# Kernel optimization log

Hardware: AMD Instinct MI355X
Metric: run time of the kernel (lower is better)

## Reference

```python
import jax, jax.numpy as jnp
import numpy as np
from jax import lax

TAU = 2.0      # LIF decay constant (source: tau = 2.0)
V_TH = 1.0     # spikingjelly LIFNode default threshold
ALPHA = 2.0    # ATan surrogate default alpha
BN_EPS = 1e-5


@jax.custom_vjp
def spike(v):
    # Heaviside with ATan surrogate gradient (spikingjelly surrogate.ATan)
    return (v >= V_TH).astype(v.dtype)

def _spike_fwd(v):
    return spike(v), v

def _spike_bwd(v, g):
    x = (jnp.pi / 2.0) * ALPHA * (v - V_TH)
    return (g * (ALPHA / 2.0) / (1.0 + x * x),)

spike.defvjp(_spike_fwd, _spike_bwd)


def lif_step(v, x):
    # leaky integrate: v += (x - (v - v_reset)) / tau, v_reset = 0
    v = v + (x - v) / TAU
    s = spike(v)
    # hard reset to 0; detach_reset=True -> stop_gradient on s in the reset path
    v = v * (1.0 - lax.stop_gradient(s))
    return v, s


def multistep_lif(x_seq):
    # x_seq: (T, ...) ; membrane state carried across T, initial v = 0
    v0 = jnp.zeros_like(x_seq[0])
    _, s_seq = lax.scan(lif_step, v0, x_seq)
    return s_seq


def setup_inputs() -> dict:
    key = jax.random.key(0)
    ks = jax.random.split(key, 3)
    bs, length, c_num, hidden = 64, 128, 32, 256
    x = jax.random.normal(ks[0], (bs, length, c_num), dtype=jnp.float32)
    conv_w = jax.random.normal(ks[1], (hidden, 1, 1, 3), dtype=jnp.float32) * 0.3
    conv_b = jnp.zeros((hidden,), jnp.float32)
    bn_gamma = jnp.ones((hidden,), jnp.float32)
    bn_beta = jnp.zeros((hidden,), jnp.float32)
    bn_mean = jnp.zeros((hidden,), jnp.float32)
    bn_var = jnp.ones((hidden,), jnp.float32)
    lin_w = jax.random.normal(ks[2], (hidden, hidden), dtype=jnp.float32) * (1.0 / np.sqrt(hidden))
    lin_b = jnp.zeros((hidden,), jnp.float32)
    return {"x": x, "conv_w": conv_w, "conv_b": conv_b, "bn_gamma": bn_gamma,
            "bn_beta": bn_beta, "bn_mean": bn_mean, "bn_var": bn_var,
            "lin_w": lin_w, "lin_b": lin_b}


def reference(x, conv_w, conv_b, bn_gamma, bn_beta, bn_mean, bn_var, lin_w, lin_b):
    bs, length, c_num = x.shape
    hidden = conv_w.shape[0]

    # ---- ConvEncoder ----
    xi = jnp.transpose(x, (0, 2, 1))[:, None]  # (bs, 1, c_num, length)
    enc = lax.conv_general_dilated(
        xi, conv_w, window_strides=(1, 1), padding=((0, 0), (1, 1)),
        dimension_numbers=("NCHW", "OIHW", "NCHW"))
    enc = enc + conv_b[None, :, None, None]
    # BatchNorm2d (eval mode, running stats)
    inv = bn_gamma * lax.rsqrt(bn_var + BN_EPS)
    enc = (enc - bn_mean[None, :, None, None]) * inv[None, :, None, None] + bn_beta[None, :, None, None]
    # multi-step LIF over channel dim T = hidden (as in source permute(1,0,2,3))
    enc = jnp.transpose(enc, (1, 0, 2, 3))          # (hidden, bs, c_num, length)
    spks_enc = multistep_lif(enc)                   # (hidden, bs, c_num, length)

    # ---- reshape to per-(bs*c_num) sequences of length `length` with feature hidden ----
    h = jnp.transpose(spks_enc, (1, 2, 3, 0)).reshape(bs * c_num, length, hidden)

    # ---- SpikeRNNCell recurrence over time (Linear + stateful LIF) ----
    def rnn_step(v, x_t):                           # x_t: (N, hidden)
        z = x_t @ lin_w.T + lin_b
        v = v + (z - v) / TAU
        s = spike(v)
        v = v * (1.0 - lax.stop_gradient(s))
        return v, s

    v0 = jnp.zeros((bs * c_num, hidden), x.dtype)
    _, s_seq = lax.scan(rnn_step, v0, jnp.transpose(h, (1, 0, 2)))  # (length, N, hidden)
    spks = s_seq[-1]                                # final-step spikes (N, hidden)

    spks = spks.reshape(bs, c_num * hidden, -1)     # (bs, c_num*hidden, 1)
    return jnp.transpose(spks, (0, 2, 1)), spks[:, :, -1]
```

## Files before the change

kernel.cpp:

```cpp
#include <hip/hip_runtime.h>
#include <stdint.h>

typedef unsigned short u16;
typedef unsigned int u32;
typedef unsigned long long u64;
typedef unsigned char u8;

typedef __attribute__((ext_vector_type(4))) int   i32x4;
typedef __attribute__((ext_vector_type(8))) int   i32x8;
typedef __attribute__((ext_vector_type(4))) float f32x4;
typedef __attribute__((ext_vector_type(2))) float f32x2;

#define OFF_SBITS 0u
#define SBITS_BYTES (2048u * 128u * 32u)
#define OFF_WQ4  (SBITS_BYTES)
#define WQ4_BYTES (2u * 32768u)
#define OFF_SCL  (OFF_WQ4 + WQ4_BYTES)

__global__ __launch_bounds__(256) void prep_enc_kernel(
    const float* __restrict__ x,
    const float* __restrict__ conv_w, const float* __restrict__ conv_b,
    const float* __restrict__ gamma,  const float* __restrict__ beta,
    const float* __restrict__ mean,   const float* __restrict__ var,
    const float* __restrict__ lin_w,  uint8_t* __restrict__ ws,
    u64* __restrict__ sbits) {
    int tid = threadIdx.x;
    int blk = blockIdx.x;
    if (blk < 256) {
        __shared__ float red[256];
        __shared__ u8 nib[256];
        int j = blk, k = tid;
        float wv = lin_w[j * 256 + k];
        red[k] = fabsf(wv);
        __syncthreads();
        #pragma unroll
        for (int s = 128; s > 0; s >>= 1) {
            if (k < s) red[k] = fmaxf(red[k], red[k + s]);
            __syncthreads();
        }
        float m = red[0];
        float S = (m > 0.f) ? 6.0f / m : 0.f;
        float v6 = wv * S;
        float av = fabsf(v6);
        int code;
        if      (av < 0.25f) code = 0;
        else if (av < 0.75f) code = 1;
        else if (av < 1.25f) code = 2;
        else if (av < 1.75f) code = 3;
        else if (av < 2.5f)  code = 4;
        else if (av < 3.5f)  code = 5;
        else if (av < 5.0f)  code = 6;
        else                 code = 7;
        nib[k] = (u8)(((v6 < 0.f && code) ? 8 : 0) | code);
        __syncthreads();
        if (k < 128) {
            u8 byte = (u8)(nib[2 * k] | (nib[2 * k + 1] << 4));
            int ks = k >> 6, kb = (k >> 4) & 3, bi = k & 15;
            (ws + OFF_WQ4)[ks * 32768 + (j * 4 + kb) * 16 + bi] = byte;
        }
        if (k == 0) ((float*)(ws + OFF_SCL))[j] = m * (1.0f / 12.0f);
    } else {
        __shared__ float4 cfl[256];
        {
            int h = tid;
            float inv = gamma[h] / sqrtf(var[h] + 1e-5f);
            float K = (conv_b[h] - mean[h]) * inv + beta[h];
            cfl[h] = make_float4(conv_w[h * 3 + 0] * inv * 0.5f,
                                 conv_w[h * 3 + 1] * inv * 0.5f,
                                 conv_w[h * 3 + 2] * inv * 0.5f, K * 0.5f);
        }
        int p = (blk - 256) * 256 + tid;
        int c = p & 31;
        int l = (p >> 5) & 127;
        int b0 = p >> 12;
        int xb = b0 * 4096 + l * 32 + c;
        float xb0 = x[xb],            xb1 = x[xb + 131072];
        float xa0 = (l > 0)   ? x[xb - 32]          : 0.f;
        float xa1 = (l > 0)   ? x[xb + 131072 - 32] : 0.f;
        float xc0 = (l < 127) ? x[xb + 32]          : 0.f;
        float xc1 = (l < 127) ? x[xb + 131072 + 32] : 0.f;
        u64* d0 = sbits + ((size_t)(b0 * 32 + c) * 128 + (size_t)l) * 4;
        u64* d1 = d0 + (size_t)1024 * 512;

        f32x2 XA = {xa0, xa1};
        f32x2 XB = {xb0, xb1};
        f32x2 XC = {xc0, xc1};
        const f32x2 half2 = {0.5f, 0.5f};

        __syncthreads();
        f32x2 v2 = {0.f, 0.f};
        u64 cur0 = 0ull, cur1 = 0ull;
        #pragma unroll 8
        for (int h = 0; h < 256; ++h) {
            float4 a = cfl[h];
            f32x2 ax = {a.x, a.x};
            f32x2 ay = {a.y, a.y};
            f32x2 az = {a.z, a.z};
            f32x2 aw = {a.w, a.w};
            f32x2 e = __builtin_elementwise_fma(az, XC, aw);
            e = __builtin_elementwise_fma(ay, XB, e);
            e = __builtin_elementwise_fma(ax, XA, e);
            v2 = __builtin_elementwise_fma(half2, v2, e);
            bool s0 = (v2.x >= 1.0f);
            bool s1 = (v2.y >= 1.0f);
            cur0 |= ((u64)(s0 ? 1u : 0u)) << (h & 63);
            cur1 |= ((u64)(s1 ? 1u : 0u)) << (h & 63);
            if ((h & 63) == 63) {
                d0[h >> 6] = cur0; d1[h >> 6] = cur1;
                cur0 = 0ull; cur1 = 0ull;
            }
            v2.x = s0 ? 0.f : v2.x;
            v2.y = s1 ? 0.f : v2.y;
        }
    }
}

__device__ __forceinline__ u32 nib_perm(u32 byte) {
    u32 t1 = byte | (byte << 6);
    u32 t2 = t1 | (t1 << 12);
    u32 sel = t2 & 0x03030303u;
    return __builtin_amdgcn_perm(0x22200200u, 0x22200200u, sel);
}

__global__ __launch_bounds__(256, 2) void gemm_scan_kernel(
    const u64* __restrict__ sbits,
    const uint4* __restrict__ wq4,
    const float* __restrict__ lin_b,
    const float* __restrict__ sclp,
    float* __restrict__ out) {
    __shared__ __align__(16) uint8_t smem[36864];
    u32* Awords = (u32*)smem;

    int tid  = threadIdx.x;
    int n    = blockIdx.x;
    int lane = tid & 63;
    int w    = tid >> 6;
    int l15  = lane & 15;
    int quad = lane >> 4;
    int lb   = w * 256 + l15 * 4 + quad;

    float bias = lin_b[tid];
    float sc   = sclp[tid];

    i32x4 bb[2][4];
    #pragma unroll
    for (int ks = 0; ks < 2; ++ks)
        #pragma unroll
        for (int nf = 0; nf < 4; ++nf)
            bb[ks][nf] = ((const i32x4*)wq4)[(size_t)(ks * 2048 + nf * 64 + lb)];

    __builtin_amdgcn_global_load_lds(
        (const __attribute__((address_space(1))) u32*)
            ((const u64*)sbits + (size_t)n * 512 + tid * 2),
        (__attribute__((address_space(3))) u32*)(smem + w * 1024), 16, 0, 0);

    f32x4 acc[8][4];
    #pragma unroll
    for (int mf = 0; mf < 8; ++mf)
        #pragma unroll
        for (int nf = 0; nf < 4; ++nf) {
            f32x4 z = {0.f, 0.f, 0.f, 0.f};
            acc[mf][nf] = z;
        }

    __syncthreads();

    u32 aw[8][2];
    #pragma unroll
    for (int mf = 0; mf < 8; ++mf)
        #pragma unroll
        for (int ks = 0; ks < 2; ++ks)
            aw[mf][ks] = Awords[(mf * 16 + l15) * 8 + ks * 4 + quad];

    i32x8 afr;
    afr[4] = 0; afr[5] = 0; afr[6] = 0; afr[7] = 0;

    #pragma unroll
    for (int ks = 0; ks < 2; ++ks) {
        i32x8 bfr[4];
        #pragma unroll
        for (int nf = 0; nf < 4; ++nf) {
            bfr[nf][0] = bb[ks][nf][0]; bfr[nf][1] = bb[ks][nf][1];
            bfr[nf][2] = bb[ks][nf][2]; bfr[nf][3] = bb[ks][nf][3];
            bfr[nf][4] = 0; bfr[nf][5] = 0; bfr[nf][6] = 0; bfr[nf][7] = 0;
        }
        #pragma unroll
        for (int mf = 0; mf < 8; ++mf) {
            u32 wbits = aw[mf][ks];
            afr[0] = (int)nib_perm(wbits & 0xFFu);
            afr[1] = (int)nib_perm((wbits >> 8) & 0xFFu);
            afr[2] = (int)nib_perm((wbits >> 16) & 0xFFu);
            afr[3] = (int)nib_perm(wbits >> 24);
            #pragma unroll
            for (int nf = 0; nf < 4; ++nf) {
                acc[mf][nf] = __builtin_amdgcn_mfma_scale_f32_16x16x128_f8f6f4(
                    afr, bfr[nf], acc[mf][nf], 4, 4,
                    0, 0x7F7F7F7F, 0, 0x7F7F7F7F);
            }
        }
    }

    __syncthreads();

    float* ZW = (float*)(smem + (size_t)w * 9216);
    float zsc = sc;
    float zbi = 0.5f * bias;
    float v = 0.f, sOut = 0.f;
    #pragma unroll
    for (int ph = 0; ph < 4; ++ph) {
        #pragma unroll
        for (int mm = 0; mm < 2; ++mm) {
            int mf = ph * 2 + mm;
            #pragma unroll
            for (int nf = 0; nf < 4; ++nf)
                *(f32x4*)(ZW + (nf * 16 + l15) * 36 + mm * 16 + quad * 4) =
                    acc[mf][nf];
        }
        float zh[32];
        #pragma unroll
        for (int g = 0; g < 8; ++g) {
            f32x4 z4 = *(const f32x4*)(ZW + lane * 36 + g * 4);
            #pragma unroll
            for (int r = 0; r < 4; ++r)
                zh[g * 4 + r] = fmaf(z4[r], zsc, zbi);
        }
        #pragma unroll
        for (int tl = 0; tl < 32; ++tl) {
            v = fmaf(0.5f, v, zh[tl]);
            bool s = (v >= 1.0f);
            if (ph == 3 && tl == 31) sOut = s ? 1.f : 0.f;
            v = s ? 0.f : v;
        }
    }
    out[(size_t)n * 256 + tid]           = sOut;
    out[524288u + (size_t)n * 256 + tid] = sOut;
}

extern "C" void kernel_launch(void* const* d_in, const int* in_sizes, int n_in,
                              void* d_out, int out_size, void* d_ws, size_t ws_size,
                              hipStream_t stream) {
    const float* x      = (const float*)d_in[0];
    const float* conv_w = (const float*)d_in[1];
    const float* conv_b = (const float*)d_in[2];
    const float* gamma  = (const float*)d_in[3];
    const float* beta   = (const float*)d_in[4];
    const float* mean   = (const float*)d_in[5];
    const float* var    = (const float*)d_in[6];
    const float* lin_w  = (const float*)d_in[7];
    const float* lin_b  = (const float*)d_in[8];
    uint8_t* ws = (uint8_t*)d_ws;
    float* out = (float*)d_out;

    hipLaunchKernelGGL(prep_enc_kernel, dim3(768), dim3(256), 0, stream,
                       x, conv_w, conv_b, gamma, beta, mean, var, lin_w,
                       ws, (u64*)(ws + OFF_SBITS));
    hipLaunchKernelGGL(gemm_scan_kernel, dim3(2048), dim3(256), 0, stream,
                       (const u64*)(ws + OFF_SBITS),
                       (const uint4*)(ws + OFF_WQ4), lin_b,
                       (const float*)(ws + OFF_SCL), out);
}
```

Baseline: 114.5 us.

## Transpose spike-bit layout to 32-bit words per hidden chunk and hand-code packed FMAs

The encoder now maps consecutive threads to consecutive time steps and writes one 32-bit spike word per 32 hidden channels. Stores become coalesced u32 writes instead of strided u64 writes. The GEMM kernel's LDS read indexing is changed to match the new layout, and the barrier moves earlier so the tile can be reused sooner. The LIF inner loop uses inline-asm v_pk_fma_f32 with op_sel broadcasts to avoid scalar splats, which adds a bit-reverse per word and ties the code to the ISA.

Result: faster. 109.5 us (-4.4%).

```diff
diff --git a/kernel.cpp b/kernel.cpp
--- a/kernel.cpp
+++ b/kernel.cpp
@@ -16,6 +16,31 @@
 #define OFF_WQ4  (SBITS_BYTES)
 #define WQ4_BYTES (2u * 32768u)
 #define OFF_SCL  (OFF_WQ4 + WQ4_BYTES)
+
+__device__ __forceinline__ f32x2 pk_fma(f32x2 a, f32x2 b, f32x2 c) {
+    f32x2 d;
+    asm("v_pk_fma_f32 %0, %1, %2, %3"
+        : "=v"(d) : "v"(a), "v"(b), "v"(c));
+    return d;
+}
+__device__ __forceinline__ f32x2 pk_fma_lw(f32x2 a, f32x2 b) {
+    f32x2 d;
+    asm("v_pk_fma_f32 %0, %1, %2, %1 op_sel:[0,0,1] op_sel_hi:[0,1,1]"
+        : "=v"(d) : "v"(a), "v"(b));
+    return d;
+}
+__device__ __forceinline__ f32x2 pk_fma_b11(f32x2 a, f32x2 b, f32x2 c) {
+    f32x2 d;
+    asm("v_pk_fma_f32 %0, %1, %2, %3 op_sel:[1,0,0] op_sel_hi:[1,1,1]"
+        : "=v"(d) : "v"(a), "v"(b), "v"(c));
+    return d;
+}
+__device__ __forceinline__ f32x2 pk_fma_b00(f32x2 a, f32x2 b, f32x2 c) {
+    f32x2 d;
+    asm("v_pk_fma_f32 %0, %1, %2, %3 op_sel:[0,0,0] op_sel_hi:[0,1,1]"
+        : "=v"(d) : "v"(a), "v"(b), "v"(c));
+    return d;
+}
 
 __global__ __launch_bounds__(256) void prep_enc_kernel(
     const float* __restrict__ x,
@@ -23,7 +48,7 @@
     const float* __restrict__ gamma,  const float* __restrict__ beta,
     const float* __restrict__ mean,   const float* __restrict__ var,
     const float* __restrict__ lin_w,  uint8_t* __restrict__ ws,
-    u64* __restrict__ sbits) {
+    u32* __restrict__ sbits) {
     int tid = threadIdx.x;
     int blk = blockIdx.x;
     if (blk < 256) {
@@ -60,18 +85,19 @@
         }
         if (k == 0) ((float*)(ws + OFF_SCL))[j] = m * (1.0f / 12.0f);
     } else {
-        __shared__ float4 cfl[256];
+        __shared__ f32x4 cfl[256];
         {
             int h = tid;
             float inv = gamma[h] / sqrtf(var[h] + 1e-5f);
             float K = (conv_b[h] - mean[h]) * inv + beta[h];
-            cfl[h] = make_float4(conv_w[h * 3 + 0] * inv * 0.5f,
-                                 conv_w[h * 3 + 1] * inv * 0.5f,
-                                 conv_w[h * 3 + 2] * inv * 0.5f, K * 0.5f);
+            f32x4 cc = {conv_w[h * 3 + 0] * inv * 0.5f,
+                        conv_w[h * 3 + 1] * inv * 0.5f,
+                        conv_w[h * 3 + 2] * inv * 0.5f, K * 0.5f};
+            cfl[h] = cc;
         }
         int p = (blk - 256) * 256 + tid;
-        int c = p & 31;
-        int l = (p >> 5) & 127;
+        int l = p & 127;
+        int c = (p >> 7) & 31;
         int b0 = p >> 12;
         int xb = b0 * 4096 + l * 32 + c;
         float xb0 = x[xb],            xb1 = x[xb + 131072];
@@ -79,38 +105,37 @@
         float xa1 = (l > 0)   ? x[xb + 131072 - 32] : 0.f;
         float xc0 = (l < 127) ? x[xb + 32]          : 0.f;
         float xc1 = (l < 127) ? x[xb + 131072 + 32] : 0.f;
-        u64* d0 = sbits + ((size_t)(b0 * 32 + c) * 128 + (size_t)l) * 4;
-        u64* d1 = d0 + (size_t)1024 * 512;
+        u32* d0 = sbits + (size_t)(b0 * 32 + c) * 1024 + l;
+        u32* d1 = d0 + (size_t)1024 * 1024;
 
         f32x2 XA = {xa0, xa1};
         f32x2 XB = {xb0, xb1};
         f32x2 XC = {xc0, xc1};
-        const f32x2 half2 = {0.5f, 0.5f};
+        const f32x2 hf2 = {0.5f, 0.5f};
 
         __syncthreads();
         f32x2 v2 = {0.f, 0.f};
-        u64 cur0 = 0ull, cur1 = 0ull;
-        #pragma unroll 8
-        for (int h = 0; h < 256; ++h) {
-            float4 a = cfl[h];
-            f32x2 ax = {a.x, a.x};
-            f32x2 ay = {a.y, a.y};
-            f32x2 az = {a.z, a.z};
-            f32x2 aw = {a.w, a.w};
-            f32x2 e = __builtin_elementwise_fma(az, XC, aw);
-            e = __builtin_elementwise_fma(ay, XB, e);
-            e = __builtin_elementwise_fma(ax, XA, e);
-            v2 = __builtin_elementwise_fma(half2, v2, e);
-            bool s0 = (v2.x >= 1.0f);
-            bool s1 = (v2.y >= 1.0f);
-            cur0 |= ((u64)(s0 ? 1u : 0u)) << (h & 63);
-            cur1 |= ((u64)(s1 ? 1u : 0u)) << (h & 63);
-            if ((h & 63) == 63) {
-                d0[h >> 6] = cur0; d1[h >> 6] = cur1;
-                cur0 = 0ull; cur1 = 0ull;
+        #pragma unroll 1
+        for (int hc = 0; hc < 8; ++hc) {
+            u32 c0 = 0, c1 = 0;
+            #pragma unroll
+            for (int k = 0; k < 32; ++k) {
+                f32x4 a4 = cfl[hc * 32 + k];
+                f32x2 p0 = __builtin_shufflevector(a4, a4, 0, 1);
+                f32x2 p1 = __builtin_shufflevector(a4, a4, 2, 3);
+                f32x2 e = pk_fma_lw(p1, XC);
+                e = pk_fma_b11(p0, XB, e);
+                e = pk_fma_b00(p0, XA, e);
+                v2 = pk_fma(hf2, v2, e);
+                bool s0 = (v2.x >= 1.0f);
+                bool s1 = (v2.y >= 1.0f);
+                c0 = (c0 << 1) | (u32)s0;
+                c1 = (c1 << 1) | (u32)s1;
+                v2.x = s0 ? 0.f : v2.x;
+                v2.y = s1 ? 0.f : v2.y;
             }
-            v2.x = s0 ? 0.f : v2.x;
-            v2.y = s1 ? 0.f : v2.y;
+            d0[hc * 128] = __builtin_bitreverse32(c0);
+            d1[hc * 128] = __builtin_bitreverse32(c1);
         }
     }
 }
@@ -123,7 +148,7 @@
 }
 
 __global__ __launch_bounds__(256, 2) void gemm_scan_kernel(
-    const u64* __restrict__ sbits,
+    const u32* __restrict__ sbits,
     const uint4* __restrict__ wq4,
     const float* __restrict__ lin_b,
     const float* __restrict__ sclp,
@@ -151,7 +176,7 @@
 
     __builtin_amdgcn_global_load_lds(
         (const __attribute__((address_space(1))) u32*)
-            ((const u64*)sbits + (size_t)n * 512 + tid * 2),
+            (sbits + (size_t)n * 1024 + tid * 4),
         (__attribute__((address_space(3))) u32*)(smem + w * 1024), 16, 0, 0);
 
     f32x4 acc[8][4];
@@ -170,7 +195,9 @@
     for (int mf = 0; mf < 8; ++mf)
         #pragma unroll
         for (int ks = 0; ks < 2; ++ks)
-            aw[mf][ks] = Awords[(mf * 16 + l15) * 8 + ks * 4 + quad];
+            aw[mf][ks] = Awords[(ks * 4 + quad) * 128 + mf * 16 + l15];
+
+    __syncthreads();
 
     i32x8 afr;
     afr[4] = 0; afr[5] = 0; afr[6] = 0; afr[7] = 0;
@@ -199,8 +226,6 @@
             }
         }
     }
-
-    __syncthreads();
 
     float* ZW = (float*)(smem + (size_t)w * 9216);
     float zsc = sc;
@@ -253,9 +278,9 @@
 
     hipLaunchKernelGGL(prep_enc_kernel, dim3(768), dim3(256), 0, stream,
                        x, conv_w, conv_b, gamma, beta, mean, var, lin_w,
-                       ws, (u64*)(ws + OFF_SBITS));
+                       ws, (u32*)(ws + OFF_SBITS));
     hipLaunchKernelGGL(gemm_scan_kernel, dim3(2048), dim3(256), 0, stream,
-                       (const u64*)(ws + OFF_SBITS),
+                       (const u32*)(ws + OFF_SBITS),
                        (const uint4*)(ws + OFF_WQ4), lin_b,
                        (const float*)(ws + OFF_SCL), out);
 }
```
